# Kernel optimization log

Measured on AMD Instinct MI355X. Metric: run time of the kernel, lower is better.

The kernel has to match this reference:

```python
import jax, jax.numpy as jnp
import numpy as np

B, N, DIM, H = 4, 2048, 1024, 16
HEAD_DIM = DIM // H
SCALE = HEAD_DIM ** -0.5


def setup_inputs() -> dict:
    key = jax.random.key(0)
    k1, k2, k3 = jax.random.split(key, 3)
    x = jax.random.normal(k1, (B, N, DIM), dtype=jnp.float32)
    w_qkv = jax.random.normal(k2, (DIM, 3 * DIM), dtype=jnp.float32) * (DIM ** -0.5)
    w_proj = jax.random.normal(k3, (DIM, DIM), dtype=jnp.float32) * (DIM ** -0.5)
    b_proj = jnp.zeros((DIM,), dtype=jnp.float32)
    return {"x": x, "w_qkv": w_qkv, "w_proj": w_proj, "b_proj": b_proj}


def reference(x, w_qkv, w_proj, b_proj):
    Bs, Ns, C = x.shape
    qkv = x @ w_qkv                       # [B, N, 3C]
    q, k, v = jnp.split(qkv, 3, axis=-1)
    # [B, N, C] -> [B, H, N, D]
    def heads(t):
        return t.reshape(Bs, Ns, H, HEAD_DIM).transpose(0, 2, 1, 3)
    q, k, v = heads(q), heads(k), heads(v)
    attn = jnp.einsum('bhnd,bhmd->bhnm', q, k) * SCALE
    attn = jax.nn.softmax(attn, axis=-1)
    out = jnp.einsum('bhnm,bhmd->bhnd', attn, v)
    out = out.transpose(0, 2, 1, 3).reshape(Bs, Ns, C)
    return out @ w_proj + b_proj
```

## Files before the change

kernel.cpp:

```cpp
#include <hip/hip_runtime.h>
#include <hip/hip_bf16.h>


typedef short bf16x8 __attribute__((ext_vector_type(8)));
typedef float f32x4  __attribute__((ext_vector_type(4)));

#define BN   4
#define SEQ  2048
#define CDIM 1024
#define NH   16
#define HD   64
#define QKVN 3072
#define MTOT 8192
#define QSCALE_LOG2E 0.18033688011112042f

static __device__ __forceinline__ unsigned short f2bf(float f){
    union { float f; unsigned int i; } v; v.f = f;
    unsigned int r = v.i + 0x7FFFu + ((v.i >> 16) & 1u);
    return (unsigned short)(r >> 16);
}

static __device__ __forceinline__ unsigned int pk2bf(float a, float b){
#if __has_builtin(__builtin_amdgcn_cvt_pk_bf16_f32)
    auto r = __builtin_amdgcn_cvt_pk_bf16_f32(a, b);
    unsigned int u; __builtin_memcpy(&u, &r, 4); return u;
#else
    return (unsigned int)f2bf(a) | ((unsigned int)f2bf(b) << 16);
#endif
}

static __device__ __forceinline__ float fast_exp2(float x){
#if __has_builtin(__builtin_amdgcn_exp2f)
    return __builtin_amdgcn_exp2f(x);
#else
    return __expf(x * 0.69314718055994531f);
#endif
}

typedef __attribute__((address_space(3))) unsigned int        as3_uint;
typedef const __attribute__((address_space(1))) unsigned int  as1_uint;
static __device__ __forceinline__ void load_lds16(
    const unsigned short* g, unsigned short* l)
{
    __builtin_amdgcn_global_load_lds((as1_uint*)g, (as3_uint*)l, 16, 0, 0);
}

#define SYNC(N) do {                                                           \
        __builtin_amdgcn_sched_barrier(0);                                     \
        asm volatile("s_waitcnt vmcnt(" #N ")" ::: "memory");                  \
        __builtin_amdgcn_s_barrier();                                          \
        __builtin_amdgcn_sched_barrier(0);                                     \
    } while (0)

#define SYNCB() do {                                                           \
        __builtin_amdgcn_sched_barrier(0);                                     \
        __builtin_amdgcn_s_barrier();                                          \
        __builtin_amdgcn_sched_barrier(0);                                     \
    } while (0)

__global__ __launch_bounds__(256) void convert_f32_bf16(
    const float* __restrict__ in, unsigned short* __restrict__ out)
{
    size_t i = ((size_t)blockIdx.x * 256 + threadIdx.x) * 8;
    f32x4 a = *(const f32x4*)(in + i);
    f32x4 b = *(const f32x4*)(in + i + 4);
    union { unsigned int u[4]; bf16x8 v; } o;
    o.u[0] = pk2bf(a[0], a[1]); o.u[1] = pk2bf(a[2], a[3]);
    o.u[2] = pk2bf(b[0], b[1]); o.u[3] = pk2bf(b[2], b[3]);
    *(bf16x8*)(out + i) = o.v;
}

__global__ __launch_bounds__(256) void transpose_f32_to_bf16(
    const float* __restrict__ in, unsigned short* __restrict__ out,
    int in_rs, int out_rs)
{
    __shared__ unsigned short tile[32][33];
    int c0 = blockIdx.x * 32, r0 = blockIdx.y * 32;
    int tx = threadIdx.x, ty = threadIdx.y;
    #pragma unroll
    for (int j = 0; j < 4; j++)
        tile[ty + 8*j][tx] = f2bf(in[(long long)(r0 + ty + 8*j) * in_rs + c0 + tx]);
    __syncthreads();
    #pragma unroll
    for (int j = 0; j < 4; j++)
        out[(long long)(c0 + ty + 8*j) * out_rs + r0 + tx] = tile[tx][ty + 8*j];
}

template<int MODE, int NX>
__global__ __launch_bounds__(256) void gemm_lds(
    const unsigned short* __restrict__ A,
    const unsigned short* __restrict__ BT,
    void* __restrict__ Cv,
    unsigned short* __restrict__ kvpack,
    const float* __restrict__ bias,
    int K, int Cstride)
{
    __shared__ unsigned short a_lds[2][4096];
    __shared__ unsigned short b_lds[2][4096];

    int tid  = threadIdx.x;
    int wave = tid >> 6, lane = tid & 63, quad = lane >> 4, l15 = lane & 15;

    int nwg = gridDim.x;
    int cpx = nwg >> 3;
    int bid = blockIdx.x;
    int swz = (bid & 7) * cpx + (bid >> 3);
    int m_blk = (swz / NX) * 128, n_blk = (swz % NX) * 128;

    int csrc = ((tid & 3) ^ ((tid >> 3) & 3)) * 8;
    int crd  = (quad ^ ((l15 >> 1) & 3)) * 8;

    const unsigned short* ag = A  + (size_t)(m_blk + (tid >> 2)) * K + csrc;
    const unsigned short* bg = BT + (size_t)(n_blk + (tid >> 2)) * K + csrc;
    const size_t row64 = (size_t)64 * K;

#define GSTAGE(BUF, T) do {                                                    \
        const unsigned short* ag_ = ag + (size_t)(T)*32;                       \
        const unsigned short* bg_ = bg + (size_t)(T)*32;                       \
        load_lds16(ag_,         &a_lds[BUF][tid*8]);                           \
        load_lds16(ag_ + row64, &a_lds[BUF][2048 + tid*8]);                    \
        load_lds16(bg_,         &b_lds[BUF][tid*8]);                           \
        load_lds16(bg_ + row64, &b_lds[BUF][2048 + tid*8]);                    \
    } while (0)

    const unsigned short* afr = &a_lds[0][((wave & 1)*64 + l15)*32 + crd];
    const unsigned short* bfr = &b_lds[0][((wave >> 1)*64 + l15)*32 + crd];

    f32x4 acc[4][4];
    #pragma unroll
    for (int i = 0; i < 4; i++)
        #pragma unroll
        for (int j = 0; j < 4; j++)
            acc[i][j] = f32x4{0.f, 0.f, 0.f, 0.f};

    int nk = K >> 5;
    GSTAGE(0, 0);
    GSTAGE(1, 1);

    for (int t = 0; t < nk; ++t) {
        if (t + 1 < nk) SYNC(4); else SYNC(0);

        int bo = (t & 1) * 4096;
        bf16x8 af[4], bfv[4];
        #pragma unroll
        for (int i = 0; i < 4; i++) af[i]  = *(const bf16x8*)(afr + bo + 16*i*32);
        #pragma unroll
        for (int i = 0; i < 4; i++) bfv[i] = *(const bf16x8*)(bfr + bo + 16*i*32);

        #pragma unroll
        for (int mi = 0; mi < 4; mi++)
            #pragma unroll
            for (int ni = 0; ni < 4; ni++)
                acc[mi][ni] = __builtin_amdgcn_mfma_f32_16x16x32_bf16(
                                  af[mi], bfv[ni], acc[mi][ni], 0, 0, 0);

        if (t + 2 < nk) {
            SYNCB();
            GSTAGE(t & 1, t + 2);
        }
    }
#undef GSTAGE

    int m0 = m_blk + (wave & 1) * 64;
    int n0 = n_blk + (wave >> 1) * 64;

    if constexpr (MODE == 0) {
        float* C = (float*)Cv;
        #pragma unroll
        for (int ni = 0; ni < 4; ni++) {
            int col = n0 + 16*ni + l15;
            float bv = bias ? bias[col] : 0.f;
            #pragma unroll
            for (int mi = 0; mi < 4; mi++)
                #pragma unroll
                for (int r = 0; r < 4; r++) {
                    int row = m0 + 16*mi + quad*4 + r;
                    C[(size_t)row * Cstride + col] = acc[mi][ni][r] + bv;
                }
        }
    } else {
        unsigned short* qkvo = (unsigned short*)Cv;
        int rg = n0 >> 10;
        if (rg == 0) {
            #pragma unroll
            for (int ni = 0; ni < 4; ni++) {
                int col = n0 + 16*ni + l15;
                #pragma unroll
                for (int mi = 0; mi < 4; mi++)
                    #pragma unroll
                    for (int r = 0; r < 4; r++) {
                        int row = m0 + 16*mi + quad*4 + r;
                        qkvo[(size_t)row * Cstride + col] =
                            f2bf(acc[mi][ni][r] * QSCALE_LOG2E);
                    }
            }
        } else if (rg == 1) {
            #pragma unroll
            for (int ni = 0; ni < 4; ni++) {
                int col = n0 + 16*ni + l15 - 1024;
                int h = col >> 6, d = col & 63;
                int quadd = (d & 31) >> 3, e = d & 7, dhi = d >> 5;
                #pragma unroll
                for (int mi = 0; mi < 4; mi++)
                    #pragma unroll
                    for (int r = 0; r < 4; r++) {
                        int row = m0 + 16*mi + quad*4 + r;
                        int b = row >> 11, t = (row & 2047) >> 5, key = row & 31;
                        int tb = (key >> 2) & 1;
                        int l15a = ((key >> 3) << 2) + (key & 3);
                        size_t addr =
                            ((size_t)(((b*16 + h)*64 + t)*8 + tb*2 + dhi))*512
                            + (size_t)(quadd*16 + l15a)*8 + e;
                        kvpack[addr] = f2bf(acc[mi][ni][r]);
                    }
            }
        } else {
            #pragma unroll
            for (int ni = 0; ni < 4; ni++) {
                int col = n0 + 16*ni + l15 - 2048;
                int h = col >> 6, d = col & 63;
                int db = d >> 4, l15v = d & 15;
                #pragma unroll
                for (int mi = 0; mi < 4; mi++) {
                    int row0 = m0 + 16*mi + quad*4;
                    int b = row0 >> 11, t = (row0 & 2047) >> 5, key0 = row0 & 31;
                    int quadv = key0 >> 3, e0 = key0 & 7;
                    size_t addr =
                        ((size_t)(((b*16 + h)*64 + t)*8 + 4 + db))*512
                        + (size_t)(quadv*16 + l15v)*8 + e0;
                    union { unsigned int u[2]; unsigned long long ull; } o;
                    o.u[0] = pk2bf(acc[mi][ni][0], acc[mi][ni][1]);
                    o.u[1] = pk2bf(acc[mi][ni][2], acc[mi][ni][3]);
                    *(unsigned long long*)(kvpack + addr) = o.ull;
                }
            }
        }
    }
}

template<int NX>
__global__ __launch_bounds__(256) void gemm_proj(
    const unsigned short* __restrict__ A,
    const unsigned short* __restrict__ BT,
    float* __restrict__ C,
    const float* __restrict__ bias,
    int K, int Cstride)
{
    __shared__ unsigned short a_lds[2][4096];
    __shared__ unsigned short b_lds[2][2048];

    int tid  = threadIdx.x;
    int wave = tid >> 6, lane = tid & 63, quad = lane >> 4, l15 = lane & 15;

    int nwg = gridDim.x;
    int cpx = nwg >> 3;
    int bid = blockIdx.x;
    int swz = (bid & 7) * cpx + (bid >> 3);
    int m_blk = (swz / NX) * 128, n_blk = (swz % NX) * 64;

    int csrc = ((tid & 3) ^ ((tid >> 3) & 3)) * 8;
    int crd  = (quad ^ ((l15 >> 1) & 3)) * 8;

    const unsigned short* ag = A  + (size_t)(m_blk + (tid >> 2)) * K + csrc;
    const unsigned short* bg = BT + (size_t)(n_blk + (tid >> 2)) * K + csrc;
    const size_t row64 = (size_t)64 * K;

#define PSTAGE(BUF, T) do {                                                    \
        const unsigned short* ag_ = ag + (size_t)(T)*32;                       \
        const unsigned short* bg_ = bg + (size_t)(T)*32;                       \
        load_lds16(ag_,         &a_lds[BUF][tid*8]);                           \
        load_lds16(ag_ + row64, &a_lds[BUF][2048 + tid*8]);                    \
        load_lds16(bg_,         &b_lds[BUF][tid*8]);                           \
    } while (0)

    const unsigned short* afr = &a_lds[0][(wave*32 + l15)*32 + crd];
    const unsigned short* bfr = &b_lds[0][l15*32 + crd];

    f32x4 acc[2][4];
    #pragma unroll
    for (int i = 0; i < 2; i++)
        #pragma unroll
        for (int j = 0; j < 4; j++)
            acc[i][j] = f32x4{0.f, 0.f, 0.f, 0.f};

    int nk = K >> 5;
    PSTAGE(0, 0);
    PSTAGE(1, 1);

    for (int t = 0; t < nk; ++t) {
        if (t + 1 < nk) SYNC(3); else SYNC(0);

        int boa = (t & 1) * 4096, bob = (t & 1) * 2048;
        bf16x8 af[2], bfv[4];
        #pragma unroll
        for (int i = 0; i < 2; i++) af[i]  = *(const bf16x8*)(afr + boa + 16*i*32);
        #pragma unroll
        for (int i = 0; i < 4; i++) bfv[i] = *(const bf16x8*)(bfr + bob + 16*i*32);

        #pragma unroll
        for (int mi = 0; mi < 2; mi++)
            #pragma unroll
            for (int ni = 0; ni < 4; ni++)
                acc[mi][ni] = __builtin_amdgcn_mfma_f32_16x16x32_bf16(
                                  af[mi], bfv[ni], acc[mi][ni], 0, 0, 0);

        if (t + 2 < nk) {
            SYNCB();
            PSTAGE(t & 1, t + 2);
        }
    }
#undef PSTAGE

    int m0 = m_blk + wave * 32;
    #pragma unroll
    for (int ni = 0; ni < 4; ni++) {
        int col = n_blk + 16*ni + l15;
        float bv = bias[col];
        #pragma unroll
        for (int mi = 0; mi < 2; mi++)
            #pragma unroll
            for (int r = 0; r < 4; r++) {
                int row = m0 + 16*mi + quad*4 + r;
                C[(size_t)row * Cstride + col] = acc[mi][ni][r] + bv;
            }
    }
}


__global__ __launch_bounds__(256, 4) void attn_kernel(
    const unsigned short* __restrict__ qkv,
    const unsigned short* __restrict__ kvpack,
    unsigned short* __restrict__ ctx)
{
    __shared__ unsigned short kvtile[4][4096];

    int tid  = threadIdx.x;
    int wave = tid >> 6, lane = tid & 63, quad = lane >> 4, l15 = lane & 15;
    int p  = blockIdx.x;
    int L  = (p & 7) * 128 + (p >> 3);
    int bh = L >> 4;
    int rb = L & 15;
    int b = bh >> 4, h = bh & 15;
    int i0 = rb * 128 + wave * 32;

    const unsigned short* qbA =
        qkv + (size_t)(b*SEQ + i0 + l15) * QKVN + h*HD + quad*8;
    const unsigned short* qbB = qbA + (size_t)16 * QKVN;
    bf16x8 qA0 = *(const bf16x8*)(qbA);
    bf16x8 qA1 = *(const bf16x8*)(qbA + 32);
    bf16x8 qB0 = *(const bf16x8*)(qbB);
    bf16x8 qB1 = *(const bf16x8*)(qbB + 32);

    const unsigned short* kvg = kvpack + (size_t)bh * 64 * 4096;

#define STAGE(BUF, T) do {                                                     \
        load_lds16(kvg + (size_t)(T)*4096 + tid*8,        &kvtile[BUF][tid*8]);\
        load_lds16(kvg + (size_t)(T)*4096 + 2048 + tid*8,                      \
                   &kvtile[BUF][2048 + tid*8]);                                \
    } while (0)

    const f32x4 zf = {0.f, 0.f, 0.f, 0.f};
    f32x4 oA0 = zf, oA1 = zf, oA2 = zf, oA3 = zf;
    f32x4 oB0 = zf, oB1 = zf, oB2 = zf, oB3 = zf;
    f32x4 lA = zf, lB = zf;

    bf16x8 ones;
    #pragma unroll
    for (int e = 0; e < 8; e++) ones[e] = (short)0x3F80;

#define ATTN_TILE(LK)                                                              \
    {                                                                              \
        bf16x8 k0a = *(const bf16x8*)((LK));                                       \
        bf16x8 k0b = *(const bf16x8*)((LK) + 512);                                 \
        bf16x8 k1a = *(const bf16x8*)((LK) + 1024);                                \
        bf16x8 k1b = *(const bf16x8*)((LK) + 1536);                                \
        bf16x8 v0  = *(const bf16x8*)((LK) + 2048);                                \
        bf16x8 v1  = *(const bf16x8*)((LK) + 2560);                                \
        bf16x8 v2  = *(const bf16x8*)((LK) + 3072);                                \
        bf16x8 v3  = *(const bf16x8*)((LK) + 3584);                                \
        __builtin_amdgcn_s_setprio(1);                                             \
        f32x4 sA0 = __builtin_amdgcn_mfma_f32_16x16x32_bf16(k0a, qA0, zf, 0,0,0);  \
        sA0 = __builtin_amdgcn_mfma_f32_16x16x32_bf16(k0b, qA1, sA0, 0,0,0);       \
        f32x4 sA1 = __builtin_amdgcn_mfma_f32_16x16x32_bf16(k1a, qA0, zf, 0,0,0);  \
        sA1 = __builtin_amdgcn_mfma_f32_16x16x32_bf16(k1b, qA1, sA1, 0,0,0);       \
        f32x4 sB0 = __builtin_amdgcn_mfma_f32_16x16x32_bf16(k0a, qB0, zf, 0,0,0);  \
        sB0 = __builtin_amdgcn_mfma_f32_16x16x32_bf16(k0b, qB1, sB0, 0,0,0);       \
        f32x4 sB1 = __builtin_amdgcn_mfma_f32_16x16x32_bf16(k1a, qB0, zf, 0,0,0);  \
        sB1 = __builtin_amdgcn_mfma_f32_16x16x32_bf16(k1b, qB1, sB1, 0,0,0);       \
        union { unsigned int u[4]; bf16x8 v; } pkA, pkB;                           \
        pkA.u[0] = pk2bf(fast_exp2(sA0[0]), fast_exp2(sA0[1]));                    \
        pkA.u[1] = pk2bf(fast_exp2(sA0[2]), fast_exp2(sA0[3]));                    \
        pkA.u[2] = pk2bf(fast_exp2(sA1[0]), fast_exp2(sA1[1]));                    \
        pkA.u[3] = pk2bf(fast_exp2(sA1[2]), fast_exp2(sA1[3]));                    \
        pkB.u[0] = pk2bf(fast_exp2(sB0[0]), fast_exp2(sB0[1]));                    \
        pkB.u[1] = pk2bf(fast_exp2(sB0[2]), fast_exp2(sB0[3]));                    \
        pkB.u[2] = pk2bf(fast_exp2(sB1[0]), fast_exp2(sB1[1]));                    \
        pkB.u[3] = pk2bf(fast_exp2(sB1[2]), fast_exp2(sB1[3]));                    \
        lA  = __builtin_amdgcn_mfma_f32_16x16x32_bf16(pkA.v, ones, lA, 0,0,0);     \
        lB  = __builtin_amdgcn_mfma_f32_16x16x32_bf16(pkB.v, ones, lB, 0,0,0);     \
        oA0 = __builtin_amdgcn_mfma_f32_16x16x32_bf16(pkA.v, v0, oA0, 0,0,0);      \
        oA1 = __builtin_amdgcn_mfma_f32_16x16x32_bf16(pkA.v, v1, oA1, 0,0,0);      \
        oA2 = __builtin_amdgcn_mfma_f32_16x16x32_bf16(pkA.v, v2, oA2, 0,0,0);      \
        oA3 = __builtin_amdgcn_mfma_f32_16x16x32_bf16(pkA.v, v3, oA3, 0,0,0);      \
        oB0 = __builtin_amdgcn_mfma_f32_16x16x32_bf16(pkB.v, v0, oB0, 0,0,0);      \
        oB1 = __builtin_amdgcn_mfma_f32_16x16x32_bf16(pkB.v, v1, oB1, 0,0,0);      \
        oB2 = __builtin_amdgcn_mfma_f32_16x16x32_bf16(pkB.v, v2, oB2, 0,0,0);      \
        oB3 = __builtin_amdgcn_mfma_f32_16x16x32_bf16(pkB.v, v3, oB3, 0,0,0);      \
        __builtin_amdgcn_s_setprio(0);                                             \
    }

    asm volatile("s_waitcnt vmcnt(0)" ::: "memory");

    STAGE(0, 0); STAGE(1, 1); STAGE(2, 2);

    const unsigned short* lds0 = &kvtile[0][lane*8];

    for (int t = 0; t < 61; ++t) {
        SYNC(4);
        STAGE((t + 3) & 3, t + 3);
        ATTN_TILE(lds0 + (t & 3) * 4096);
    }
    SYNC(4); ATTN_TILE(lds0 + 1 * 4096);
    SYNC(2); ATTN_TILE(lds0 + 2 * 4096);
    SYNC(0); ATTN_TILE(lds0 + 3 * 4096);

    #pragma unroll
    for (int r = 0; r < 4; r++) {
        float invA = 1.f / lA[r];
        float invB = 1.f / lB[r];
        int rowA = b*SEQ + i0 + quad*4 + r;
        size_t baseA = (size_t)rowA * CDIM + h*HD + l15;
        size_t baseB = baseA + (size_t)16 * CDIM;
        ctx[baseA]      = f2bf(oA0[r] * invA);
        ctx[baseA + 16] = f2bf(oA1[r] * invA);
        ctx[baseA + 32] = f2bf(oA2[r] * invA);
        ctx[baseA + 48] = f2bf(oA3[r] * invA);
        ctx[baseB]      = f2bf(oB0[r] * invB);
        ctx[baseB + 16] = f2bf(oB1[r] * invB);
        ctx[baseB + 32] = f2bf(oB2[r] * invB);
        ctx[baseB + 48] = f2bf(oB3[r] * invB);
    }
#undef STAGE
#undef ATTN_TILE
}

extern "C" void kernel_launch(void* const* d_in, const int* in_sizes, int n_in,
                              void* d_out, int out_size, void* d_ws, size_t ws_size,
                              hipStream_t stream)
{
    const float* x      = (const float*)d_in[0];
    const float* w_qkv  = (const float*)d_in[1];
    const float* w_proj = (const float*)d_in[2];
    const float* b_proj = (const float*)d_in[3];
    float* out = (float*)d_out;

    char* ws = (char*)d_ws;
    unsigned short* qkv    = (unsigned short*)(ws);
    unsigned short* ctx    = (unsigned short*)(ws + 50331648);
    unsigned short* xb     = ctx;
    unsigned short* kvpack = (unsigned short*)(ws + 67108864);
    unsigned short* wqkvT  = (unsigned short*)(ws + 100663296);
    unsigned short* wprojT = (unsigned short*)(ws + 106954752);

    dim3 tb(32, 8);
    transpose_f32_to_bf16<<<dim3(QKVN/32, CDIM/32), tb, 0, stream>>>(
        w_qkv, wqkvT, QKVN, CDIM);
    transpose_f32_to_bf16<<<dim3(CDIM/32, CDIM/32), tb, 0, stream>>>(
        w_proj, wprojT, CDIM, CDIM);

    convert_f32_bf16<<<dim3(MTOT*CDIM/2048), 256, 0, stream>>>(x, xb);

    gemm_lds<1, QKVN/128><<<dim3((QKVN/128)*(MTOT/128)), 256, 0, stream>>>(
        xb, wqkvT, qkv, kvpack, nullptr, CDIM, QKVN);

    attn_kernel<<<dim3(BN * NH * (SEQ/128)), 256, 0, stream>>>(
        qkv, kvpack, ctx);

    gemm_proj<CDIM/64><<<dim3((CDIM/64)*(MTOT/128)), 256, 0, stream>>>(
        ctx, wprojT, out, b_proj, CDIM, CDIM);
}
```

Measured before the change: 263.3 us.

## Software-pipeline attention softmax with PV across tiles and fuse prep kernels

The attention loop is restructured so each iteration computes QK^T for the current KV tile while doing the P·V MFMAs for the previous tile's packed probabilities. This overlaps the exp/pack VALU work with matrix-core work, using double-buffered V and P registers. The three input-prep launches (x conversion and two weight transposes) are merged into one kernel to cut launch overhead. The occupancy hint of 4 blocks per SM is dropped from launch_bounds and barriers now also wait on lgkmcnt. Together these raise register pressure and may lower occupancy.

```diff
diff --git a/kernel.cpp b/kernel.cpp
--- a/kernel.cpp
+++ b/kernel.cpp
@@ -52,31 +52,47 @@
         __builtin_amdgcn_sched_barrier(0);                                     \
     } while (0)
 
+#define SYNCA(N) do {                                                          \
+        __builtin_amdgcn_sched_barrier(0);                                     \
+        asm volatile("s_waitcnt vmcnt(" #N ") lgkmcnt(0)" ::: "memory");       \
+        __builtin_amdgcn_s_barrier();                                          \
+        __builtin_amdgcn_sched_barrier(0);                                     \
+    } while (0)
+
 #define SYNCB() do {                                                           \
         __builtin_amdgcn_sched_barrier(0);                                     \
         __builtin_amdgcn_s_barrier();                                          \
         __builtin_amdgcn_sched_barrier(0);                                     \
     } while (0)
 
-__global__ __launch_bounds__(256) void convert_f32_bf16(
-    const float* __restrict__ in, unsigned short* __restrict__ out)
-{
-    size_t i = ((size_t)blockIdx.x * 256 + threadIdx.x) * 8;
-    f32x4 a = *(const f32x4*)(in + i);
-    f32x4 b = *(const f32x4*)(in + i + 4);
-    union { unsigned int u[4]; bf16x8 v; } o;
-    o.u[0] = pk2bf(a[0], a[1]); o.u[1] = pk2bf(a[2], a[3]);
-    o.u[2] = pk2bf(b[0], b[1]); o.u[3] = pk2bf(b[2], b[3]);
-    *(bf16x8*)(out + i) = o.v;
-}
-
-__global__ __launch_bounds__(256) void transpose_f32_to_bf16(
-    const float* __restrict__ in, unsigned short* __restrict__ out,
-    int in_rs, int out_rs)
+__global__ __launch_bounds__(256) void prep_kernel(
+    const float* __restrict__ x, const float* __restrict__ w_qkv,
+    const float* __restrict__ w_proj, unsigned short* __restrict__ xb,
+    unsigned short* __restrict__ wqkvT, unsigned short* __restrict__ wprojT)
 {
     __shared__ unsigned short tile[32][33];
-    int c0 = blockIdx.x * 32, r0 = blockIdx.y * 32;
-    int tx = threadIdx.x, ty = threadIdx.y;
+    int bid = blockIdx.x, tid = threadIdx.x;
+    if (bid < 4096) {
+        size_t i = ((size_t)bid * 256 + tid) * 8;
+        f32x4 a = *(const f32x4*)(x + i);
+        f32x4 b = *(const f32x4*)(x + i + 4);
+        union { unsigned int u[4]; bf16x8 v; } o;
+        o.u[0] = pk2bf(a[0], a[1]); o.u[1] = pk2bf(a[2], a[3]);
+        o.u[2] = pk2bf(b[0], b[1]); o.u[3] = pk2bf(b[2], b[3]);
+        *(bf16x8*)(xb + i) = o.v;
+        return;
+    }
+    int tx = tid & 31, ty = tid >> 5;
+    const float* in; unsigned short* out; int in_rs, out_rs, c0, r0;
+    if (bid < 4096 + 3072) {
+        int b = bid - 4096;
+        c0 = (b % 96) * 32; r0 = (b / 96) * 32;
+        in = w_qkv; out = wqkvT; in_rs = QKVN; out_rs = CDIM;
+    } else {
+        int b = bid - 7168;
+        c0 = (b & 31) * 32; r0 = (b >> 5) * 32;
+        in = w_proj; out = wprojT; in_rs = CDIM; out_rs = CDIM;
+    }
     #pragma unroll
     for (int j = 0; j < 4; j++)
         tile[ty + 8*j][tx] = f2bf(in[(long long)(r0 + ty + 8*j) * in_rs + c0 + tx]);
@@ -327,7 +343,16 @@
 }
 
 
-__global__ __launch_bounds__(256, 4) void attn_kernel(
+static __device__ __forceinline__ bf16x8 sm_pack(f32x4 s0, f32x4 s1){
+    union { unsigned int u[4]; bf16x8 v; } pk;
+    pk.u[0] = pk2bf(fast_exp2(s0[0]), fast_exp2(s0[1]));
+    pk.u[1] = pk2bf(fast_exp2(s0[2]), fast_exp2(s0[3]));
+    pk.u[2] = pk2bf(fast_exp2(s1[0]), fast_exp2(s1[1]));
+    pk.u[3] = pk2bf(fast_exp2(s1[2]), fast_exp2(s1[3]));
+    return pk.v;
+}
+
+__global__ __launch_bounds__(256) void attn_kernel(
     const unsigned short* __restrict__ qkv,
     const unsigned short* __restrict__ kvpack,
     unsigned short* __restrict__ ctx)
@@ -368,16 +393,31 @@
     #pragma unroll
     for (int e = 0; e < 8; e++) ones[e] = (short)0x3F80;
 
-#define ATTN_TILE(LK)                                                              \
+    bf16x8 va0, va1, va2, va3, vb0, vb1, vb2, vb3;
+    bf16x8 pkAa, pkBa, pkAb, pkBb;
+
+#define PVSTEP(PKA, PKB, V0, V1, V2, V3)                                           \
+        lA  = __builtin_amdgcn_mfma_f32_16x16x32_bf16(PKA, ones, lA, 0,0,0);       \
+        lB  = __builtin_amdgcn_mfma_f32_16x16x32_bf16(PKB, ones, lB, 0,0,0);       \
+        oA0 = __builtin_amdgcn_mfma_f32_16x16x32_bf16(PKA, V0, oA0, 0,0,0);        \
+        oA1 = __builtin_amdgcn_mfma_f32_16x16x32_bf16(PKA, V1, oA1, 0,0,0);        \
+        oA2 = __builtin_amdgcn_mfma_f32_16x16x32_bf16(PKA, V2, oA2, 0,0,0);        \
+        oA3 = __builtin_amdgcn_mfma_f32_16x16x32_bf16(PKA, V3, oA3, 0,0,0);        \
+        oB0 = __builtin_amdgcn_mfma_f32_16x16x32_bf16(PKB, V0, oB0, 0,0,0);        \
+        oB1 = __builtin_amdgcn_mfma_f32_16x16x32_bf16(PKB, V1, oB1, 0,0,0);        \
+        oB2 = __builtin_amdgcn_mfma_f32_16x16x32_bf16(PKB, V2, oB2, 0,0,0);        \
+        oB3 = __builtin_amdgcn_mfma_f32_16x16x32_bf16(PKB, V3, oB3, 0,0,0);
+
+#define STEP(LK, VC0,VC1,VC2,VC3, PKA_C,PKB_C, VP0,VP1,VP2,VP3, PKA_P,PKB_P)       \
     {                                                                              \
         bf16x8 k0a = *(const bf16x8*)((LK));                                       \
         bf16x8 k0b = *(const bf16x8*)((LK) + 512);                                 \
         bf16x8 k1a = *(const bf16x8*)((LK) + 1024);                                \
         bf16x8 k1b = *(const bf16x8*)((LK) + 1536);                                \
-        bf16x8 v0  = *(const bf16x8*)((LK) + 2048);                                \
-        bf16x8 v1  = *(const bf16x8*)((LK) + 2560);                                \
-        bf16x8 v2  = *(const bf16x8*)((LK) + 3072);                                \
-        bf16x8 v3  = *(const bf16x8*)((LK) + 3584);                                \
+        VC0 = *(const bf16x8*)((LK) + 2048);                                       \
+        VC1 = *(const bf16x8*)((LK) + 2560);                                       \
+        VC2 = *(const bf16x8*)((LK) + 3072);                                       \
+        VC3 = *(const bf16x8*)((LK) + 3584);                                       \
         __builtin_amdgcn_s_setprio(1);                                             \
         f32x4 sA0 = __builtin_amdgcn_mfma_f32_16x16x32_bf16(k0a, qA0, zf, 0,0,0);  \
         sA0 = __builtin_amdgcn_mfma_f32_16x16x32_bf16(k0b, qA1, sA0, 0,0,0);       \
@@ -387,26 +427,34 @@
         sB0 = __builtin_amdgcn_mfma_f32_16x16x32_bf16(k0b, qB1, sB0, 0,0,0);       \
         f32x4 sB1 = __builtin_amdgcn_mfma_f32_16x16x32_bf16(k1a, qB0, zf, 0,0,0);  \
         sB1 = __builtin_amdgcn_mfma_f32_16x16x32_bf16(k1b, qB1, sB1, 0,0,0);       \
-        union { unsigned int u[4]; bf16x8 v; } pkA, pkB;                           \
-        pkA.u[0] = pk2bf(fast_exp2(sA0[0]), fast_exp2(sA0[1]));                    \
-        pkA.u[1] = pk2bf(fast_exp2(sA0[2]), fast_exp2(sA0[3]));                    \
-        pkA.u[2] = pk2bf(fast_exp2(sA1[0]), fast_exp2(sA1[1]));                    \
-        pkA.u[3] = pk2bf(fast_exp2(sA1[2]), fast_exp2(sA1[3]));                    \
-        pkB.u[0] = pk2bf(fast_exp2(sB0[0]), fast_exp2(sB0[1]));                    \
-        pkB.u[1] = pk2bf(fast_exp2(sB0[2]), fast_exp2(sB0[3]));                    \
-        pkB.u[2] = pk2bf(fast_exp2(sB1[0]), fast_exp2(sB1[1]));                    \
-        pkB.u[3] = pk2bf(fast_exp2(sB1[2]), fast_exp2(sB1[3]));                    \
-        lA  = __builtin_amdgcn_mfma_f32_16x16x32_bf16(pkA.v, ones, lA, 0,0,0);     \
-        lB  = __builtin_amdgcn_mfma_f32_16x16x32_bf16(pkB.v, ones, lB, 0,0,0);     \
-        oA0 = __builtin_amdgcn_mfma_f32_16x16x32_bf16(pkA.v, v0, oA0, 0,0,0);      \
-        oA1 = __builtin_amdgcn_mfma_f32_16x16x32_bf16(pkA.v, v1, oA1, 0,0,0);      \
-        oA2 = __builtin_amdgcn_mfma_f32_16x16x32_bf16(pkA.v, v2, oA2, 0,0,0);      \
-        oA3 = __builtin_amdgcn_mfma_f32_16x16x32_bf16(pkA.v, v3, oA3, 0,0,0);      \
-        oB0 = __builtin_amdgcn_mfma_f32_16x16x32_bf16(pkB.v, v0, oB0, 0,0,0);      \
-        oB1 = __builtin_amdgcn_mfma_f32_16x16x32_bf16(pkB.v, v1, oB1, 0,0,0);      \
-        oB2 = __builtin_amdgcn_mfma_f32_16x16x32_bf16(pkB.v, v2, oB2, 0,0,0);      \
-        oB3 = __builtin_amdgcn_mfma_f32_16x16x32_bf16(pkB.v, v3, oB3, 0,0,0);      \
+        PVSTEP(PKA_P, PKB_P, VP0, VP1, VP2, VP3);                                  \
         __builtin_amdgcn_s_setprio(0);                                             \
+        PKA_C = sm_pack(sA0, sA1);                                                 \
+        PKB_C = sm_pack(sB0, sB1);                                                 \
+    }
+
+#define STEP0(LK, VC0,VC1,VC2,VC3, PKA_C,PKB_C)                                    \
+    {                                                                              \
+        bf16x8 k0a = *(const bf16x8*)((LK));                                       \
+        bf16x8 k0b = *(const bf16x8*)((LK) + 512);                                 \
+        bf16x8 k1a = *(const bf16x8*)((LK) + 1024);                                \
+        bf16x8 k1b = *(const bf16x8*)((LK) + 1536);                                \
+        VC0 = *(const bf16x8*)((LK) + 2048);                                       \
+        VC1 = *(const bf16x8*)((LK) + 2560);                                       \
+        VC2 = *(const bf16x8*)((LK) + 3072);                                       \
+        VC3 = *(const bf16x8*)((LK) + 3584);                                       \
+        __builtin_amdgcn_s_setprio(1);                                             \
+        f32x4 sA0 = __builtin_amdgcn_mfma_f32_16x16x32_bf16(k0a, qA0, zf, 0,0,0);  \
+        sA0 = __builtin_amdgcn_mfma_f32_16x16x32_bf16(k0b, qA1, sA0, 0,0,0);       \
+        f32x4 sA1 = __builtin_amdgcn_mfma_f32_16x16x32_bf16(k1a, qA0, zf, 0,0,0);  \
+        sA1 = __builtin_amdgcn_mfma_f32_16x16x32_bf16(k1b, qA1, sA1, 0,0,0);       \
+        f32x4 sB0 = __builtin_amdgcn_mfma_f32_16x16x32_bf16(k0a, qB0, zf, 0,0,0);  \
+        sB0 = __builtin_amdgcn_mfma_f32_16x16x32_bf16(k0b, qB1, sB0, 0,0,0);       \
+        f32x4 sB1 = __builtin_amdgcn_mfma_f32_16x16x32_bf16(k1a, qB0, zf, 0,0,0);  \
+        sB1 = __builtin_amdgcn_mfma_f32_16x16x32_bf16(k1b, qB1, sB1, 0,0,0);       \
+        __builtin_amdgcn_s_setprio(0);                                             \
+        PKA_C = sm_pack(sA0, sA1);                                                 \
+        PKB_C = sm_pack(sB0, sB1);                                                 \
     }
 
     asm volatile("s_waitcnt vmcnt(0)" ::: "memory");
@@ -415,14 +463,24 @@
 
     const unsigned short* lds0 = &kvtile[0][lane*8];
 
-    for (int t = 0; t < 61; ++t) {
-        SYNC(4);
-        STAGE((t + 3) & 3, t + 3);
-        ATTN_TILE(lds0 + (t & 3) * 4096);
-    }
-    SYNC(4); ATTN_TILE(lds0 + 1 * 4096);
-    SYNC(2); ATTN_TILE(lds0 + 2 * 4096);
-    SYNC(0); ATTN_TILE(lds0 + 3 * 4096);
+    SYNCA(4); STAGE(3, 3);
+    STEP0(lds0 + 0*4096, va0,va1,va2,va3, pkAa,pkBa);
+
+    for (int t = 1; t < 61; t += 2) {
+        SYNCA(4); STAGE((t + 3) & 3, t + 3);
+        STEP(lds0 + (t & 3) * 4096,
+             vb0,vb1,vb2,vb3, pkAb,pkBb, va0,va1,va2,va3, pkAa,pkBa);
+        SYNCA(4); STAGE((t + 4) & 3, t + 4);
+        STEP(lds0 + ((t + 1) & 3) * 4096,
+             va0,va1,va2,va3, pkAa,pkBa, vb0,vb1,vb2,vb3, pkAb,pkBb);
+    }
+    SYNCA(4); STEP(lds0 + 1*4096, vb0,vb1,vb2,vb3, pkAb,pkBb,
+                   va0,va1,va2,va3, pkAa,pkBa);
+    SYNCA(2); STEP(lds0 + 2*4096, va0,va1,va2,va3, pkAa,pkBa,
+                   vb0,vb1,vb2,vb3, pkAb,pkBb);
+    SYNCA(0); STEP(lds0 + 3*4096, vb0,vb1,vb2,vb3, pkAb,pkBb,
+                   va0,va1,va2,va3, pkAa,pkBa);
+    PVSTEP(pkAb, pkBb, vb0, vb1, vb2, vb3);
 
     #pragma unroll
     for (int r = 0; r < 4; r++) {
@@ -441,7 +499,9 @@
         ctx[baseB + 48] = f2bf(oB3[r] * invB);
     }
 #undef STAGE
-#undef ATTN_TILE
+#undef STEP
+#undef STEP0
+#undef PVSTEP
 }
 
 extern "C" void kernel_launch(void* const* d_in, const int* in_sizes, int n_in,
@@ -462,13 +522,8 @@
     unsigned short* wqkvT  = (unsigned short*)(ws + 100663296);
     unsigned short* wprojT = (unsigned short*)(ws + 106954752);
 
-    dim3 tb(32, 8);
-    transpose_f32_to_bf16<<<dim3(QKVN/32, CDIM/32), tb, 0, stream>>>(
-        w_qkv, wqkvT, QKVN, CDIM);
-    transpose_f32_to_bf16<<<dim3(CDIM/32, CDIM/32), tb, 0, stream>>>(
-        w_proj, wprojT, CDIM, CDIM);
-
-    convert_f32_bf16<<<dim3(MTOT*CDIM/2048), 256, 0, stream>>>(x, xb);
+    prep_kernel<<<dim3(8192), 256, 0, stream>>>(
+        x, w_qkv, w_proj, xb, wqkvT, wprojT);
 
     gemm_lds<1, QKVN/128><<<dim3((QKVN/128)*(MTOT/128)), 256, 0, stream>>>(
         xb, wqkvT, qkv, kvpack, nullptr, CDIM, QKVN);
```

Result: slower. 290.7 us (+10.4%).
